# Optimization experiments

Hardware: AMD Instinct MI355X
Metric: run time of the kernel (lower is better)

Reference implementation:

```python
import jax, jax.numpy as jnp
import numpy as np

N = 100000
E = 1600000
IN_C, HID_C, OUT_C = 128, 128, 64


def setup_inputs() -> dict:
    key = jax.random.key(0)
    ks = jax.random.split(key, 8)
    x = jax.random.normal(ks[0], (N, IN_C), dtype=jnp.float32)
    edge_index = jax.random.randint(ks[1], (2, E), 0, N, dtype=jnp.int64)
    # Glorot-ish init for the 3 GCNConv linear weights + zero biases (PyG default)
    def glorot(k, fan_in, fan_out):
        s = jnp.sqrt(6.0 / (fan_in + fan_out))
        return jax.random.uniform(k, (fan_in, fan_out), jnp.float32, -s, s)
    return {
        "x": x,
        "edge_index": edge_index,
        "W1": glorot(ks[2], IN_C, HID_C), "b1": jnp.zeros((HID_C,), jnp.float32),
        "W2": glorot(ks[3], HID_C, HID_C), "b2": jnp.zeros((HID_C,), jnp.float32),
        "W3": glorot(ks[4], HID_C, OUT_C), "b3": jnp.zeros((OUT_C,), jnp.float32),
    }


def _gcn_norm(edge_index, num_nodes):
    # add self loops, compute D^-1/2 (A+I) D^-1/2 edge coefficients (PyG gcn_norm)
    loop = jnp.arange(num_nodes, dtype=edge_index.dtype)
    src = jnp.concatenate([edge_index[0], loop])  # [E+N]
    dst = jnp.concatenate([edge_index[1], loop])
    w = jnp.ones_like(src, dtype=jnp.float32)
    deg = jax.ops.segment_sum(w, dst, num_segments=num_nodes)
    dinv = jnp.where(deg > 0, jax.lax.rsqrt(deg), 0.0)
    norm = dinv[src] * dinv[dst]  # [E+N]
    return src, dst, norm


def _gcn_layer(x, src, dst, norm, W, b, num_nodes):
    h = x @ W                                   # [N, out]
    msg = h[src] * norm[:, None]                # gather + scale, [E+N, out]
    agg = jax.ops.segment_sum(msg, dst, num_segments=num_nodes)  # scatter-add
    return agg + b


def reference(x, edge_index, W1, b1, W2, b2, W3, b3):
    src, dst, norm = _gcn_norm(edge_index, N)
    h = jax.nn.relu(_gcn_layer(x, src, dst, norm, W1, b1, N))
    h = jax.nn.relu(_gcn_layer(h, src, dst, norm, W2, b2, N))
    h = _gcn_layer(h, src, dst, norm, W3, b3, N)
    return jax.nn.log_softmax(h, axis=-1)  # [N, OUT_C]
```

## Files before the change

### kernel.cpp

```cpp
#include <hip/hip_runtime.h>
#include <hip/hip_bf16.h>


constexpr int N_NODES = 100000;
constexpr int E_EDGES = 1600000;
constexpr int NB = (N_NODES + 127) / 128;
constexpr int BCAP = 2560;
constexpr int CHUNK = 4096;
constexpr int NCHUNK = (E_EDGES + CHUNK - 1) / CHUNK;

typedef short bf16x8 __attribute__((ext_vector_type(8)));
typedef float f32x4 __attribute__((ext_vector_type(4)));

__device__ __forceinline__ unsigned short f2bf(float f) {
    unsigned u = __float_as_uint(f);
    unsigned r = (u + 0x7fff + ((u >> 16) & 1)) >> 16;
    return (unsigned short)r;
}
__device__ __forceinline__ float bf_lo(unsigned u) { return __uint_as_float(u << 16); }
__device__ __forceinline__ float bf_hi(unsigned u) { return __uint_as_float(u & 0xffff0000u); }
__device__ __forceinline__ unsigned pack2bf(float lo, float hi) {
    return (unsigned)f2bf(lo) | ((unsigned)f2bf(hi) << 16);
}

__device__ __forceinline__ int get_idx(const void* ei, int use64, long long pos) {
    if (use64) return (int)((const long long*)ei)[pos];
    return ((const int*)ei)[pos];
}

__global__ void prep_wt_kernel(const float* __restrict__ W1, const float* __restrict__ W2,
                               const float* __restrict__ W3,
                               unsigned short* __restrict__ WT1,
                               unsigned short* __restrict__ WT2,
                               unsigned short* __restrict__ WT3,
                               const int* __restrict__ ei32, int* __restrict__ flag) {
    const int b = blockIdx.x;
    if (b == 3) {
        if (threadIdx.x == 0) {
            int ok64 = 1;
#pragma unroll
            for (int i = 1; i < 64; i += 2) ok64 &= (ei32[i] == 0);
            *flag = ok64;
        }
        return;
    }
    const float* W = (b == 0) ? W1 : (b == 1) ? W2 : W3;
    unsigned short* WT = (b == 0) ? WT1 : (b == 1) ? WT2 : WT3;
    const int COUT = (b == 2) ? 64 : 128;
    for (int i = threadIdx.x; i < COUT * 128; i += blockDim.x) {
        int c = i >> 7;
        int k = i & 127;
        WT[c * 128 + k] = f2bf(W[k * COUT + c]);
    }
}

__global__ __launch_bounds__(256) void scatter_direct(
    const void* __restrict__ ei, const int* __restrict__ flag,
    int* __restrict__ cursorPad, unsigned* __restrict__ pairs) {
    __shared__ int h[NB];
    __shared__ int base[NB];
    __shared__ unsigned dstb[CHUNK];
    const int t = threadIdx.x;
    const int use64 = *flag;
    const int e0 = blockIdx.x * CHUNK;
    const int e1 = min(E_EDGES, e0 + CHUNK);

    for (int i = t; i < NB; i += 256) h[i] = 0;
    __syncthreads();
    for (int e = e0 + t; e < e1; e += 256) {
        unsigned d = (unsigned)get_idx(ei, use64, (long long)E_EDGES + e);
        dstb[e - e0] = d;
        atomicAdd(&h[d >> 7], 1);
    }
    __syncthreads();
    for (int i = t; i < NB; i += 256) {
        int c = h[i];
        if (c) base[i] = atomicAdd(&cursorPad[i * 16], c);
        h[i] = 0;
    }
    __syncthreads();
    for (int e = e0 + t; e < e1; e += 256) {
        unsigned s = (unsigned)get_idx(ei, use64, e);
        unsigned d = dstb[e - e0];
        int b = d >> 7;
        int r = base[b] + atomicAdd(&h[b], 1);
        if (r < BCAP) pairs[(unsigned)b * BCAP + r] = (s << 7) | (d & 127u);
    }
}

__global__ __launch_bounds__(256) void fine_sort_kernel(
    const unsigned* __restrict__ pairs, const int* __restrict__ cursorPad,
    int* __restrict__ csr, int* __restrict__ rowptr, int* __restrict__ deg,
    float* __restrict__ dinv) {
    __shared__ int h[128];
    __shared__ int rp[128];
    __shared__ int sc[128];
    const int t = threadIdx.x;
    const int b = blockIdx.x;
    const int base = b * BCAP;
    const int cnt = min(cursorPad[b * 16], BCAP);

    if (t < 128) h[t] = 0;
    __syncthreads();
    for (int i = t; i < cnt; i += 256) {
        unsigned p = pairs[base + i];
        atomicAdd(&h[p & 127u], 1);
    }
    __syncthreads();
    int v = (t < 128) ? h[t] : 0;
    if (t < 128) sc[t] = v;
    __syncthreads();
    int incl = v;
    for (int off = 1; off < 128; off <<= 1) {
        int add = (t >= off && t < 128) ? sc[t - off] : 0;
        __syncthreads();
        if (t < 128) {
            incl += add;
            sc[t] = incl;
        }
        __syncthreads();
    }
    if (t < 128) {
        rp[t] = incl - v;
        int node = b * 128 + t;
        if (node < N_NODES) {
            rowptr[node] = base + incl - v;
            deg[node] = v;
            dinv[node] = rsqrtf((float)(v + 1));
        }
        h[t] = 0;
    }
    __syncthreads();
    for (int i = t; i < cnt; i += 256) {
        unsigned p = pairs[base + i];
        int l = (int)(p & 127u);
        int r = atomicAdd(&h[l], 1);
        csr[base + rp[l] + r] = (int)(p >> 7);
    }
}

template <int COUT>
__global__ __launch_bounds__(256) void gemm_mfma_f32(const float* __restrict__ X,
                                                     const unsigned short* __restrict__ WT,
                                                     const float* __restrict__ dinv,
                                                     unsigned short* __restrict__ H) {
    constexpr int NT = COUT / 16;
    __shared__ short Albs[64 * 128];
    __shared__ short Wlds[COUT * 128];

    const int t = threadIdx.x;
    const int row0 = blockIdx.x * 64;

    for (int i = t; i < COUT * 16; i += 256) {
        int n = i >> 4, k8 = i & 15;
        bf16x8 v = *(const bf16x8*)&WT[n * 128 + k8 * 8];
        *(bf16x8*)&Wlds[(k8 * COUT + n) * 8] = v;
    }
    for (int i = t; i < 1024; i += 256) {
        int m = i >> 4, k8 = i & 15;
        int gr = min(row0 + m, N_NODES - 1);
        const float* p = &X[(size_t)gr * 128 + k8 * 8];
        float4 f0 = *(const float4*)p;
        float4 f1 = *(const float4*)(p + 4);
        bf16x8 v;
        v[0] = (short)f2bf(f0.x); v[1] = (short)f2bf(f0.y);
        v[2] = (short)f2bf(f0.z); v[3] = (short)f2bf(f0.w);
        v[4] = (short)f2bf(f1.x); v[5] = (short)f2bf(f1.y);
        v[6] = (short)f2bf(f1.z); v[7] = (short)f2bf(f1.w);
        int u = ((m >> 4) * 16 + (k8 >> 2) * 4 + (k8 & 3)) * 16 + (m & 15);
        *(bf16x8*)&Albs[u * 8] = v;
    }
    __syncthreads();

    const int lane = t & 63;
    const int wv = t >> 6;
    const int l15 = lane & 15;
    const int quad = lane >> 4;

    f32x4 acc[NT];
#pragma unroll
    for (int ct = 0; ct < NT; ct++) acc[ct] = (f32x4){0.f, 0.f, 0.f, 0.f};

#pragma unroll
    for (int kcg = 0; kcg < 4; kcg++) {
        bf16x8 a = *(const bf16x8*)&Albs[((wv * 16 + kcg * 4 + quad) * 16 + l15) * 8];
#pragma unroll
        for (int ct = 0; ct < NT; ct++) {
            bf16x8 b = *(const bf16x8*)&Wlds[((kcg * 4 + quad) * COUT + ct * 16 + l15) * 8];
            acc[ct] = __builtin_amdgcn_mfma_f32_16x16x32_bf16(a, b, acc[ct], 0, 0, 0);
        }
    }

    const int m0 = row0 + wv * 16;
#pragma unroll
    for (int r = 0; r < 4; r++) {
        int m = m0 + quad * 4 + r;
        if (m < N_NODES) {
            float dv = dinv[m];
#pragma unroll
            for (int ct = 0; ct < NT; ct++)
                H[(size_t)m * COUT + ct * 16 + l15] = f2bf(acc[ct][r] * dv);
        } else if (m == N_NODES) {
#pragma unroll
            for (int ct = 0; ct < NT; ct++)
                H[(size_t)m * COUT + ct * 16 + l15] = 0;
        }
    }
}

template <int COUT>
__global__ __launch_bounds__(256) void gemm_mfma_bf16(const unsigned short* __restrict__ X,
                                                      const unsigned short* __restrict__ WT,
                                                      const float* __restrict__ dinv,
                                                      unsigned short* __restrict__ H) {
    constexpr int NT = COUT / 16;
    __shared__ short Albs[64 * 128];
    __shared__ short Wlds[COUT * 128];

    const int t = threadIdx.x;
    const int row0 = blockIdx.x * 64;

    for (int i = t; i < COUT * 16; i += 256) {
        int n = i >> 4, k8 = i & 15;
        bf16x8 v = *(const bf16x8*)&WT[n * 128 + k8 * 8];
        *(bf16x8*)&Wlds[(k8 * COUT + n) * 8] = v;
    }
    for (int i = t; i < 1024; i += 256) {
        int m = i >> 4, k8 = i & 15;
        int gr = min(row0 + m, N_NODES - 1);
        bf16x8 v = *(const bf16x8*)&X[(size_t)gr * 128 + k8 * 8];
        int u = ((m >> 4) * 16 + (k8 >> 2) * 4 + (k8 & 3)) * 16 + (m & 15);
        *(bf16x8*)&Albs[u * 8] = v;
    }
    __syncthreads();

    const int lane = t & 63;
    const int wv = t >> 6;
    const int l15 = lane & 15;
    const int quad = lane >> 4;

    f32x4 acc[NT];
#pragma unroll
    for (int ct = 0; ct < NT; ct++) acc[ct] = (f32x4){0.f, 0.f, 0.f, 0.f};

#pragma unroll
    for (int kcg = 0; kcg < 4; kcg++) {
        bf16x8 a = *(const bf16x8*)&Albs[((wv * 16 + kcg * 4 + quad) * 16 + l15) * 8];
#pragma unroll
        for (int ct = 0; ct < NT; ct++) {
            bf16x8 b = *(const bf16x8*)&Wlds[((kcg * 4 + quad) * COUT + ct * 16 + l15) * 8];
            acc[ct] = __builtin_amdgcn_mfma_f32_16x16x32_bf16(a, b, acc[ct], 0, 0, 0);
        }
    }

    const int m0 = row0 + wv * 16;
#pragma unroll
    for (int r = 0; r < 4; r++) {
        int m = m0 + quad * 4 + r;
        if (m < N_NODES) {
            float dv = dinv[m];
#pragma unroll
            for (int ct = 0; ct < NT; ct++)
                H[(size_t)m * COUT + ct * 16 + l15] = f2bf(acc[ct][r] * dv);
        } else if (m == N_NODES) {
#pragma unroll
            for (int ct = 0; ct < NT; ct++)
                H[(size_t)m * COUT + ct * 16 + l15] = 0;
        }
    }
}

__global__ __launch_bounds__(256) void aggregate128_pair(
    const unsigned short* __restrict__ Hb, const int* __restrict__ rowptr,
    const int* __restrict__ deg, const int* __restrict__ csr,
    const float* __restrict__ dinv, const float* __restrict__ bias,
    unsigned short* __restrict__ out) {
    const int lane = threadIdx.x & 63;
    const int wv = threadIdx.x >> 6;
    const int li = lane & 31;
    const int half = lane >> 5;
    const int n = blockIdx.x * 8 + wv * 2 + half;
    const unsigned li8 = (unsigned)li * 8u;
    const char* Hc = (const char*)Hb;

    uint2 s = *(const uint2*)(Hc + (size_t)n * 256u + li8);
    float a0 = bf_lo(s.x), a1 = bf_hi(s.x), a2 = bf_lo(s.y), a3 = bf_hi(s.y);

    const int start = rowptr[n];
    const int dc = deg[n];
    const int dmax = max(dc, __shfl_xor(dc, 32));

    for (int eb = 0; eb < dmax; eb += 32) {
        int myidx = N_NODES;
        if (eb + li < dc) myidx = csr[start + eb + li];
        const int jmax = min(32, dmax - eb);
        int j = 0;
        for (; j + 16 <= jmax; j += 16) {
            int idx[16];
            uint2 u[16];
#pragma unroll
            for (int q = 0; q < 16; q++) idx[q] = __shfl(myidx, j + q, 32);
#pragma unroll
            for (int q = 0; q < 16; q++)
                u[q] = *(const uint2*)(Hc + (((unsigned)idx[q] << 8) + li8));
#pragma unroll
            for (int q = 0; q < 16; q++) {
                a0 += bf_lo(u[q].x); a1 += bf_hi(u[q].x);
                a2 += bf_lo(u[q].y); a3 += bf_hi(u[q].y);
            }
        }
        for (; j + 8 <= jmax; j += 8) {
            int idx[8];
            uint2 u[8];
#pragma unroll
            for (int q = 0; q < 8; q++) idx[q] = __shfl(myidx, j + q, 32);
#pragma unroll
            for (int q = 0; q < 8; q++)
                u[q] = *(const uint2*)(Hc + (((unsigned)idx[q] << 8) + li8));
#pragma unroll
            for (int q = 0; q < 8; q++) {
                a0 += bf_lo(u[q].x); a1 += bf_hi(u[q].x);
                a2 += bf_lo(u[q].y); a3 += bf_hi(u[q].y);
            }
        }
        for (; j + 4 <= jmax; j += 4) {
            int idx[4];
            uint2 u[4];
#pragma unroll
            for (int q = 0; q < 4; q++) idx[q] = __shfl(myidx, j + q, 32);
#pragma unroll
            for (int q = 0; q < 4; q++)
                u[q] = *(const uint2*)(Hc + (((unsigned)idx[q] << 8) + li8));
#pragma unroll
            for (int q = 0; q < 4; q++) {
                a0 += bf_lo(u[q].x); a1 += bf_hi(u[q].x);
                a2 += bf_lo(u[q].y); a3 += bf_hi(u[q].y);
            }
        }
        for (; j < jmax; j++) {
            int i0 = __shfl(myidx, j, 32);
            uint2 u0 = *(const uint2*)(Hc + (((unsigned)i0 << 8) + li8));
            a0 += bf_lo(u0.x); a1 += bf_hi(u0.x);
            a2 += bf_lo(u0.y); a3 += bf_hi(u0.y);
        }
    }

    const float dn = dinv[n];
    float4 bv = *(const float4*)((const char*)bias + li * 16);
    uint2 o;
    o.x = pack2bf(fmaxf(a0 * dn + bv.x, 0.f), fmaxf(a1 * dn + bv.y, 0.f));
    o.y = pack2bf(fmaxf(a2 * dn + bv.z, 0.f), fmaxf(a3 * dn + bv.w, 0.f));
    *(uint2*)((char*)out + (size_t)n * 256 + li * 8) = o;
}

__global__ __launch_bounds__(256) void aggregate64_lsm_pair(
    const unsigned short* __restrict__ Hb, const int* __restrict__ rowptr,
    const int* __restrict__ deg, const int* __restrict__ csr,
    const float* __restrict__ dinv, const float* __restrict__ bias,
    float* __restrict__ out) {
    const int lane = threadIdx.x & 63;
    const int wv = threadIdx.x >> 6;
    const int li = lane & 31;
    const int half = lane >> 5;
    const int n = blockIdx.x * 8 + wv * 2 + half;
    const unsigned li4 = (unsigned)li * 4u;
    const char* Hc = (const char*)Hb;

    unsigned s = *(const unsigned*)(Hc + (size_t)n * 128u + li4);
    float a0 = bf_lo(s), a1 = bf_hi(s);

    const int start = rowptr[n];
    const int dc = deg[n];
    const int dmax = max(dc, __shfl_xor(dc, 32));

    for (int eb = 0; eb < dmax; eb += 32) {
        int myidx = N_NODES;
        if (eb + li < dc) myidx = csr[start + eb + li];
        const int jmax = min(32, dmax - eb);
        int j = 0;
        for (; j + 16 <= jmax; j += 16) {
            int idx[16];
            unsigned u[16];
#pragma unroll
            for (int q = 0; q < 16; q++) idx[q] = __shfl(myidx, j + q, 32);
#pragma unroll
            for (int q = 0; q < 16; q++)
                u[q] = *(const unsigned*)(Hc + (((unsigned)idx[q] << 7) + li4));
#pragma unroll
            for (int q = 0; q < 16; q++) { a0 += bf_lo(u[q]); a1 += bf_hi(u[q]); }
        }
        for (; j + 8 <= jmax; j += 8) {
            int idx[8];
            unsigned u[8];
#pragma unroll
            for (int q = 0; q < 8; q++) idx[q] = __shfl(myidx, j + q, 32);
#pragma unroll
            for (int q = 0; q < 8; q++)
                u[q] = *(const unsigned*)(Hc + (((unsigned)idx[q] << 7) + li4));
#pragma unroll
            for (int q = 0; q < 8; q++) { a0 += bf_lo(u[q]); a1 += bf_hi(u[q]); }
        }
        for (; j + 4 <= jmax; j += 4) {
            int idx[4];
            unsigned u[4];
#pragma unroll
            for (int q = 0; q < 4; q++) idx[q] = __shfl(myidx, j + q, 32);
#pragma unroll
            for (int q = 0; q < 4; q++)
                u[q] = *(const unsigned*)(Hc + (((unsigned)idx[q] << 7) + li4));
#pragma unroll
            for (int q = 0; q < 4; q++) { a0 += bf_lo(u[q]); a1 += bf_hi(u[q]); }
        }
        for (; j < jmax; j++) {
            int i0 = __shfl(myidx, j, 32);
            unsigned u0 = *(const unsigned*)(Hc + (((unsigned)i0 << 7) + li4));
            a0 += bf_lo(u0); a1 += bf_hi(u0);
        }
    }

    const float dn = dinv[n];
    float2 bv = *(const float2*)((const char*)bias + li * 8);
    float v0 = a0 * dn + bv.x;
    float v1 = a1 * dn + bv.y;

    float m = fmaxf(v0, v1);
#pragma unroll
    for (int off = 16; off; off >>= 1) m = fmaxf(m, __shfl_xor(m, off));
    float e = expf(v0 - m) + expf(v1 - m);
#pragma unroll
    for (int off = 16; off; off >>= 1) e += __shfl_xor(e, off);
    float lse = m + logf(e);
    float2 o = make_float2(v0 - lse, v1 - lse);
    *(float2*)((char*)out + (size_t)n * 256 + li * 8) = o;
}

extern "C" void kernel_launch(void* const* d_in, const int* in_sizes, int n_in,
                              void* d_out, int out_size, void* d_ws, size_t ws_size,
                              hipStream_t stream) {
    const float* x = (const float*)d_in[0];
    const void* ei = d_in[1];
    const float* W1 = (const float*)d_in[2];
    const float* b1 = (const float*)d_in[3];
    const float* W2 = (const float*)d_in[4];
    const float* b2 = (const float*)d_in[5];
    const float* W3 = (const float*)d_in[6];
    const float* b3 = (const float*)d_in[7];
    float* out = (float*)d_out;

    char* w = (char*)d_ws;
    size_t off = 0;
    auto take = [&](size_t bytes) {
        char* p = w + off;
        off = (off + bytes + 255) & ~(size_t)255;
        return p;
    };
    int* flag = (int*)take(4);
    int* cursorPad = (int*)take((size_t)NB * 64);
    int* deg = (int*)take((size_t)N_NODES * 4);
    int* rowptr = (int*)take((size_t)N_NODES * 4);
    float* dinv = (float*)take((size_t)N_NODES * 4);
    int* csr = (int*)take((size_t)NB * BCAP * 4);
    unsigned short* WT1 = (unsigned short*)take(128 * 128 * 2);
    unsigned short* WT2 = (unsigned short*)take(128 * 128 * 2);
    unsigned short* WT3 = (unsigned short*)take(64 * 128 * 2);
    unsigned short* A = (unsigned short*)take((size_t)(N_NODES + 1) * 128 * 2);
    unsigned short* B = (unsigned short*)take((size_t)N_NODES * 128 * 2);
    unsigned* pairs = (unsigned*)A;

    hipMemsetAsync(cursorPad, 0, (size_t)NB * 64, stream);
    prep_wt_kernel<<<4, 256, 0, stream>>>(W1, W2, W3, WT1, WT2, WT3, (const int*)ei, flag);
    scatter_direct<<<NCHUNK, 256, 0, stream>>>(ei, flag, cursorPad, pairs);
    fine_sort_kernel<<<NB, 256, 0, stream>>>(pairs, cursorPad, csr, rowptr, deg, dinv);

    const int gg = (N_NODES + 63) / 64 + 1;
    const int gagg = N_NODES / 8;

    gemm_mfma_f32<128><<<gg, 256, 0, stream>>>(x, WT1, dinv, A);
    aggregate128_pair<<<gagg, 256, 0, stream>>>(A, rowptr, deg, csr, dinv, b1, B);
    gemm_mfma_bf16<128><<<gg, 256, 0, stream>>>(B, WT2, dinv, A);
    aggregate128_pair<<<gagg, 256, 0, stream>>>(A, rowptr, deg, csr, dinv, b2, B);
    gemm_mfma_bf16<64><<<gg, 256, 0, stream>>>(B, WT3, dinv, A);
    aggregate64_lsm_pair<<<gagg, 256, 0, stream>>>(A, rowptr, deg, csr, dinv, b3, out);
}
```

Baseline: 366.4 us.

## Aggregate one node per wavefront with edge-parallel slots and 16-byte gathers

The aggregation kernels now give each 64-lane wavefront a single node instead of two. The wavefront is split into slots that each gather different neighbor rows with 16-byte loads, and the partial sums are combined with cross-lane shuffle reductions. This aims to raise memory-level parallelism and cut the load divergence caused by pairing two nodes of unequal degree. It costs extra shuffle reductions and idle lanes in the epilogue, plus twice as many blocks. The cursor memset is also folded into the weight-prep kernel, removing one launch.

Result: slower. 387.3 us (+5.7%).

```diff
diff --git a/kernel.cpp b/kernel.cpp
--- a/kernel.cpp
+++ b/kernel.cpp
@@ -22,6 +22,12 @@
 __device__ __forceinline__ unsigned pack2bf(float lo, float hi) {
     return (unsigned)f2bf(lo) | ((unsigned)f2bf(hi) << 16);
 }
+__device__ __forceinline__ void acc8(float* a, uint4 u) {
+    a[0] += bf_lo(u.x); a[1] += bf_hi(u.x);
+    a[2] += bf_lo(u.y); a[3] += bf_hi(u.y);
+    a[4] += bf_lo(u.z); a[5] += bf_hi(u.z);
+    a[6] += bf_lo(u.w); a[7] += bf_hi(u.w);
+}
 
 __device__ __forceinline__ int get_idx(const void* ei, int use64, long long pos) {
     if (use64) return (int)((const long long*)ei)[pos];
@@ -33,9 +39,11 @@
                                unsigned short* __restrict__ WT1,
                                unsigned short* __restrict__ WT2,
                                unsigned short* __restrict__ WT3,
-                               const int* __restrict__ ei32, int* __restrict__ flag) {
+                               const int* __restrict__ ei32, int* __restrict__ flag,
+                               int* __restrict__ cursorPad) {
     const int b = blockIdx.x;
     if (b == 3) {
+        for (int i = threadIdx.x; i < NB * 16; i += blockDim.x) cursorPad[i] = 0;
         if (threadIdx.x == 0) {
             int ok64 = 1;
 #pragma unroll
@@ -270,168 +278,150 @@
     }
 }
 
-__global__ __launch_bounds__(256) void aggregate128_pair(
+__global__ __launch_bounds__(256) void aggregate128_quad(
     const unsigned short* __restrict__ Hb, const int* __restrict__ rowptr,
     const int* __restrict__ deg, const int* __restrict__ csr,
     const float* __restrict__ dinv, const float* __restrict__ bias,
     unsigned short* __restrict__ out) {
     const int lane = threadIdx.x & 63;
-    const int wv = threadIdx.x >> 6;
-    const int li = lane & 31;
-    const int half = lane >> 5;
-    const int n = blockIdx.x * 8 + wv * 2 + half;
-    const unsigned li8 = (unsigned)li * 8u;
+    const int n = blockIdx.x * 4 + (threadIdx.x >> 6);
+    const int li = lane & 15;
+    const int slot = lane >> 4;
+    const unsigned off16 = (unsigned)li * 16u;
     const char* Hc = (const char*)Hb;
 
-    uint2 s = *(const uint2*)(Hc + (size_t)n * 256u + li8);
-    float a0 = bf_lo(s.x), a1 = bf_hi(s.x), a2 = bf_lo(s.y), a3 = bf_hi(s.y);
+    float a[8];
+#pragma unroll
+    for (int q = 0; q < 8; q++) a[q] = 0.f;
 
     const int start = rowptr[n];
     const int dc = deg[n];
-    const int dmax = max(dc, __shfl_xor(dc, 32));
-
-    for (int eb = 0; eb < dmax; eb += 32) {
+
+    for (int eb = 0; eb < dc; eb += 64) {
         int myidx = N_NODES;
-        if (eb + li < dc) myidx = csr[start + eb + li];
-        const int jmax = min(32, dmax - eb);
+        if (eb + lane < dc) myidx = csr[start + eb + lane];
+        const int cnt = min(64, dc - eb);
+        const int jmax = (cnt + 3) >> 2;
         int j = 0;
-        for (; j + 16 <= jmax; j += 16) {
-            int idx[16];
-            uint2 u[16];
-#pragma unroll
-            for (int q = 0; q < 16; q++) idx[q] = __shfl(myidx, j + q, 32);
-#pragma unroll
-            for (int q = 0; q < 16; q++)
-                u[q] = *(const uint2*)(Hc + (((unsigned)idx[q] << 8) + li8));
-#pragma unroll
-            for (int q = 0; q < 16; q++) {
-                a0 += bf_lo(u[q].x); a1 += bf_hi(u[q].x);
-                a2 += bf_lo(u[q].y); a3 += bf_hi(u[q].y);
-            }
-        }
-        for (; j + 8 <= jmax; j += 8) {
-            int idx[8];
-            uint2 u[8];
-#pragma unroll
-            for (int q = 0; q < 8; q++) idx[q] = __shfl(myidx, j + q, 32);
-#pragma unroll
-            for (int q = 0; q < 8; q++)
-                u[q] = *(const uint2*)(Hc + (((unsigned)idx[q] << 8) + li8));
-#pragma unroll
-            for (int q = 0; q < 8; q++) {
-                a0 += bf_lo(u[q].x); a1 += bf_hi(u[q].x);
-                a2 += bf_lo(u[q].y); a3 += bf_hi(u[q].y);
-            }
-        }
         for (; j + 4 <= jmax; j += 4) {
             int idx[4];
-            uint2 u[4];
-#pragma unroll
-            for (int q = 0; q < 4; q++) idx[q] = __shfl(myidx, j + q, 32);
+            uint4 u[4];
+#pragma unroll
+            for (int q = 0; q < 4; q++) idx[q] = __shfl(myidx, (j + q) * 4 + slot, 64);
 #pragma unroll
             for (int q = 0; q < 4; q++)
-                u[q] = *(const uint2*)(Hc + (((unsigned)idx[q] << 8) + li8));
-#pragma unroll
-            for (int q = 0; q < 4; q++) {
-                a0 += bf_lo(u[q].x); a1 += bf_hi(u[q].x);
-                a2 += bf_lo(u[q].y); a3 += bf_hi(u[q].y);
-            }
+                u[q] = *(const uint4*)(Hc + (((unsigned)idx[q] << 8) + off16));
+#pragma unroll
+            for (int q = 0; q < 4; q++) acc8(a, u[q]);
         }
         for (; j < jmax; j++) {
-            int i0 = __shfl(myidx, j, 32);
-            uint2 u0 = *(const uint2*)(Hc + (((unsigned)i0 << 8) + li8));
-            a0 += bf_lo(u0.x); a1 += bf_hi(u0.x);
-            a2 += bf_lo(u0.y); a3 += bf_hi(u0.y);
-        }
-    }
-
-    const float dn = dinv[n];
-    float4 bv = *(const float4*)((const char*)bias + li * 16);
-    uint2 o;
-    o.x = pack2bf(fmaxf(a0 * dn + bv.x, 0.f), fmaxf(a1 * dn + bv.y, 0.f));
-    o.y = pack2bf(fmaxf(a2 * dn + bv.z, 0.f), fmaxf(a3 * dn + bv.w, 0.f));
-    *(uint2*)((char*)out + (size_t)n * 256 + li * 8) = o;
-}
-
-__global__ __launch_bounds__(256) void aggregate64_lsm_pair(
+            int i0 = __shfl(myidx, j * 4 + slot, 64);
+            uint4 u0 = *(const uint4*)(Hc + (((unsigned)i0 << 8) + off16));
+            acc8(a, u0);
+        }
+    }
+
+#pragma unroll
+    for (int q = 0; q < 8; q++) {
+        a[q] += __shfl_xor(a[q], 32);
+        a[q] += __shfl_xor(a[q], 16);
+    }
+
+    if (lane < 16) {
+        uint4 s = *(const uint4*)(Hc + (size_t)n * 256u + off16);
+        acc8(a, s);
+        const float dn = dinv[n];
+        float4 b0 = *(const float4*)(bias + li * 8);
+        float4 b1 = *(const float4*)(bias + li * 8 + 4);
+        uint4 o;
+        o.x = pack2bf(fmaxf(a[0] * dn + b0.x, 0.f), fmaxf(a[1] * dn + b0.y, 0.f));
+        o.y = pack2bf(fmaxf(a[2] * dn + b0.z, 0.f), fmaxf(a[3] * dn + b0.w, 0.f));
+        o.z = pack2bf(fmaxf(a[4] * dn + b1.x, 0.f), fmaxf(a[5] * dn + b1.y, 0.f));
+        o.w = pack2bf(fmaxf(a[6] * dn + b1.z, 0.f), fmaxf(a[7] * dn + b1.w, 0.f));
+        *(uint4*)((char*)out + (size_t)n * 256u + off16) = o;
+    }
+}
+
+__global__ __launch_bounds__(256) void aggregate64_lsm_quad(
     const unsigned short* __restrict__ Hb, const int* __restrict__ rowptr,
     const int* __restrict__ deg, const int* __restrict__ csr,
     const float* __restrict__ dinv, const float* __restrict__ bias,
     float* __restrict__ out) {
     const int lane = threadIdx.x & 63;
-    const int wv = threadIdx.x >> 6;
-    const int li = lane & 31;
-    const int half = lane >> 5;
-    const int n = blockIdx.x * 8 + wv * 2 + half;
-    const unsigned li4 = (unsigned)li * 4u;
+    const int n = blockIdx.x * 4 + (threadIdx.x >> 6);
+    const int li = lane & 7;
+    const int slot = lane >> 3;
+    const unsigned off16 = (unsigned)li * 16u;
     const char* Hc = (const char*)Hb;
 
-    unsigned s = *(const unsigned*)(Hc + (size_t)n * 128u + li4);
-    float a0 = bf_lo(s), a1 = bf_hi(s);
+    float a[8];
+#pragma unroll
+    for (int q = 0; q < 8; q++) a[q] = 0.f;
 
     const int start = rowptr[n];
     const int dc = deg[n];
-    const int dmax = max(dc, __shfl_xor(dc, 32));
-
-    for (int eb = 0; eb < dmax; eb += 32) {
+
+    for (int eb = 0; eb < dc; eb += 64) {
         int myidx = N_NODES;
-        if (eb + li < dc) myidx = csr[start + eb + li];
-        const int jmax = min(32, dmax - eb);
+        if (eb + lane < dc) myidx = csr[start + eb + lane];
+        const int cnt = min(64, dc - eb);
+        const int jmax = (cnt + 7) >> 3;
         int j = 0;
-        for (; j + 16 <= jmax; j += 16) {
-            int idx[16];
-            unsigned u[16];
-#pragma unroll
-            for (int q = 0; q < 16; q++) idx[q] = __shfl(myidx, j + q, 32);
-#pragma unroll
-            for (int q = 0; q < 16; q++)
-                u[q] = *(const unsigned*)(Hc + (((unsigned)idx[q] << 7) + li4));
-#pragma unroll
-            for (int q = 0; q < 16; q++) { a0 += bf_lo(u[q]); a1 += bf_hi(u[q]); }
-        }
-        for (; j + 8 <= jmax; j += 8) {
-            int idx[8];
-            unsigned u[8];
-#pragma unroll
-            for (int q = 0; q < 8; q++) idx[q] = __shfl(myidx, j + q, 32);
-#pragma unroll
-            for (int q = 0; q < 8; q++)
-                u[q] = *(const unsigned*)(Hc + (((unsigned)idx[q] << 7) + li4));
-#pragma unroll
-            for (int q = 0; q < 8; q++) { a0 += bf_lo(u[q]); a1 += bf_hi(u[q]); }
-        }
         for (; j + 4 <= jmax; j += 4) {
             int idx[4];
-            unsigned u[4];
-#pragma unroll
-            for (int q = 0; q < 4; q++) idx[q] = __shfl(myidx, j + q, 32);
+            uint4 u[4];
+#pragma unroll
+            for (int q = 0; q < 4; q++) idx[q] = __shfl(myidx, (j + q) * 8 + slot, 64);
 #pragma unroll
             for (int q = 0; q < 4; q++)
-                u[q] = *(const unsigned*)(Hc + (((unsigned)idx[q] << 7) + li4));
-#pragma unroll
-            for (int q = 0; q < 4; q++) { a0 += bf_lo(u[q]); a1 += bf_hi(u[q]); }
+                u[q] = *(const uint4*)(Hc + (((unsigned)idx[q] << 7) + off16));
+#pragma unroll
+            for (int q = 0; q < 4; q++) acc8(a, u[q]);
         }
         for (; j < jmax; j++) {
-            int i0 = __shfl(myidx, j, 32);
-            unsigned u0 = *(const unsigned*)(Hc + (((unsigned)i0 << 7) + li4));
-            a0 += bf_lo(u0); a1 += bf_hi(u0);
-        }
-    }
-
-    const float dn = dinv[n];
-    float2 bv = *(const float2*)((const char*)bias + li * 8);
-    float v0 = a0 * dn + bv.x;
-    float v1 = a1 * dn + bv.y;
-
-    float m = fmaxf(v0, v1);
-#pragma unroll
-    for (int off = 16; off; off >>= 1) m = fmaxf(m, __shfl_xor(m, off));
-    float e = expf(v0 - m) + expf(v1 - m);
-#pragma unroll
-    for (int off = 16; off; off >>= 1) e += __shfl_xor(e, off);
-    float lse = m + logf(e);
-    float2 o = make_float2(v0 - lse, v1 - lse);
-    *(float2*)((char*)out + (size_t)n * 256 + li * 8) = o;
+            int i0 = __shfl(myidx, j * 8 + slot, 64);
+            uint4 u0 = *(const uint4*)(Hc + (((unsigned)i0 << 7) + off16));
+            acc8(a, u0);
+        }
+    }
+
+#pragma unroll
+    for (int q = 0; q < 8; q++) {
+        a[q] += __shfl_xor(a[q], 32);
+        a[q] += __shfl_xor(a[q], 16);
+        a[q] += __shfl_xor(a[q], 8);
+    }
+
+    if (lane < 8) {
+        uint4 s = *(const uint4*)(Hc + (size_t)n * 128u + off16);
+        acc8(a, s);
+        const float dn = dinv[n];
+        float4 b0 = *(const float4*)(bias + li * 8);
+        float4 b1 = *(const float4*)(bias + li * 8 + 4);
+        float v[8];
+        v[0] = a[0] * dn + b0.x; v[1] = a[1] * dn + b0.y;
+        v[2] = a[2] * dn + b0.z; v[3] = a[3] * dn + b0.w;
+        v[4] = a[4] * dn + b1.x; v[5] = a[5] * dn + b1.y;
+        v[6] = a[6] * dn + b1.z; v[7] = a[7] * dn + b1.w;
+
+        float m = v[0];
+#pragma unroll
+        for (int q = 1; q < 8; q++) m = fmaxf(m, v[q]);
+#pragma unroll
+        for (int off = 4; off; off >>= 1) m = fmaxf(m, __shfl_xor(m, off, 8));
+        float e = 0.f;
+#pragma unroll
+        for (int q = 0; q < 8; q++) e += expf(v[q] - m);
+#pragma unroll
+        for (int off = 4; off; off >>= 1) e += __shfl_xor(e, off, 8);
+        float lse = m + logf(e);
+
+        float* op = out + (size_t)n * 64 + li * 8;
+        float4 o0 = make_float4(v[0] - lse, v[1] - lse, v[2] - lse, v[3] - lse);
+        float4 o1 = make_float4(v[4] - lse, v[5] - lse, v[6] - lse, v[7] - lse);
+        *(float4*)op = o0;
+        *(float4*)(op + 4) = o1;
+    }
 }
 
 extern "C" void kernel_launch(void* const* d_in, const int* in_sizes, int n_in,
@@ -467,18 +457,18 @@
     unsigned short* B = (unsigned short*)take((size_t)N_NODES * 128 * 2);
     unsigned* pairs = (unsigned*)A;
 
-    hipMemsetAsync(cursorPad, 0, (size_t)NB * 64, stream);
-    prep_wt_kernel<<<4, 256, 0, stream>>>(W1, W2, W3, WT1, WT2, WT3, (const int*)ei, flag);
+    prep_wt_kernel<<<4, 256, 0, stream>>>(W1, W2, W3, WT1, WT2, WT3,
+                                          (const int*)ei, flag, cursorPad);
     scatter_direct<<<NCHUNK, 256, 0, stream>>>(ei, flag, cursorPad, pairs);
     fine_sort_kernel<<<NB, 256, 0, stream>>>(pairs, cursorPad, csr, rowptr, deg, dinv);
 
     const int gg = (N_NODES + 63) / 64 + 1;
-    const int gagg = N_NODES / 8;
+    const int gagg = N_NODES / 4;
 
     gemm_mfma_f32<128><<<gg, 256, 0, stream>>>(x, WT1, dinv, A);
-    aggregate128_pair<<<gagg, 256, 0, stream>>>(A, rowptr, deg, csr, dinv, b1, B);
+    aggregate128_quad<<<gagg, 256, 0, stream>>>(A, rowptr, deg, csr, dinv, b1, B);
     gemm_mfma_bf16<128><<<gg, 256, 0, stream>>>(B, WT2, dinv, A);
-    aggregate128_pair<<<gagg, 256, 0, stream>>>(A, rowptr, deg, csr, dinv, b2, B);
+    aggregate128_quad<<<gagg, 256, 0, stream>>>(A, rowptr, deg, csr, dinv, b2, B);
     gemm_mfma_bf16<64><<<gg, 256, 0, stream>>>(B, WT3, dinv, A);
-    aggregate64_lsm_pair<<<gagg, 256, 0, stream>>>(A, rowptr, deg, csr, dinv, b3, out);
-}
+    aggregate64_lsm_quad<<<gagg, 256, 0, stream>>>(A, rowptr, deg, csr, dinv, b3, out);
+}
```
